# Optimization experiments

Hardware: AMD Instinct MI355X
Metric: run time of the kernel (lower is better)

The kernel has to match this reference:

```python
import jax, jax.numpy as jnp
import numpy as np

N = 100000          # nodes
E = 800000          # edges
H = 32              # hidden_features
L = 4               # num_layers
HS = 32             # hidden_edge_scores
EPS_BN = 1e-5
EPS_AGG = 1e-6


def _bn(x, g, b):
    # training-mode batch norm over the node/edge (batch) axis
    mu = jnp.mean(x, axis=0)
    var = jnp.var(x, axis=0)
    return (x - mu) * jax.lax.rsqrt(var + EPS_BN) * g + b


def setup_inputs() -> dict:
    key = jax.random.key(0)
    ks = jax.random.split(key, 24)
    rn = lambda k, s, sc=0.1: jax.random.normal(k, s, dtype=jnp.float32) * sc
    return {
        "x": rn(ks[0], (N, 1), 1.0),
        "e": rn(ks[1], (E, 1), 1.0),
        "edge_index": jax.random.randint(ks[2], (2, E), 0, N),
        # input projections
        "pe_w": rn(ks[3], (1, H)), "pe_b": rn(ks[4], (H,)),
        "ed_w": rn(ks[5], (1, H)), "ed_b": rn(ks[6], (H,)),
        # per-layer GatedGCN weights, stacked over layers
        "A_w": rn(ks[7], (L, H, H)), "A_b": rn(ks[8], (L, H)),
        "B_w": rn(ks[9], (L, H, H)), "B_b": rn(ks[10], (L, H)),
        "C_w": rn(ks[11], (L, H, H)), "C_b": rn(ks[12], (L, H)),
        "U_w": rn(ks[13], (L, H, H)), "U_b": rn(ks[14], (L, H)),
        "V_w": rn(ks[15], (L, H, H)), "V_b": rn(ks[16], (L, H)),
        # batch-norm affine params
        "bn_h_g": jnp.ones((L, H), jnp.float32), "bn_h_b": jnp.zeros((L, H), jnp.float32),
        "bn_e_g": jnp.ones((L, H), jnp.float32), "bn_e_b": jnp.zeros((L, H), jnp.float32),
        # score predictor: concat(src_h, dst_h, e) -> HS -> 1
        "W1_w": rn(ks[17], (3 * H, HS)), "W1_b": rn(ks[18], (HS,)),
        "W2_w": rn(ks[19], (HS, 1)), "W2_b": rn(ks[20], (1,)),
    }


def reference(x, e, edge_index, pe_w, pe_b, ed_w, ed_b,
              A_w, A_b, B_w, B_b, C_w, C_b, U_w, U_b, V_w, V_b,
              bn_h_g, bn_h_b, bn_e_g, bn_e_b, W1_w, W1_b, W2_w, W2_b):
    src, dst = edge_index[0], edge_index[1]
    h = x @ pe_w + pe_b          # [N, H]
    e = e @ ed_w + ed_b          # [E, H]
    n = h.shape[0]
    for l in range(L):
        Ah = h @ A_w[l] + A_b[l]
        Bh = h @ B_w[l] + B_b[l]
        Ce = e @ C_w[l] + C_b[l]
        Uh = h @ U_w[l] + U_b[l]
        Vh = h @ V_w[l] + V_b[l]
        # edge update: gather node features to edges
        e_new = Ah[dst] + Bh[src] + Ce               # [E, H]
        sigma = jax.nn.sigmoid(e_new)                # edge gates
        # gated mean aggregation: scatter-add to dst nodes
        num = jax.ops.segment_sum(sigma * Vh[src], dst, num_segments=n)
        den = jax.ops.segment_sum(sigma, dst, num_segments=n)
        h_new = Uh + num / (den + EPS_AGG)           # [N, H]
        # BN -> ReLU -> residual
        h = h + jax.nn.relu(_bn(h_new, bn_h_g[l], bn_h_b[l]))
        e = e + jax.nn.relu(_bn(e_new, bn_e_g[l], bn_e_b[l]))
    # score predictor over edges
    z = jnp.concatenate([h[src], h[dst], e], axis=1)  # [E, 3H]
    scores = jax.nn.relu(z @ W1_w + W1_b) @ W2_w + W2_b  # [E, 1]
    return scores
```

## Files before the change

### kernel.cpp

```cpp
#include <hip/hip_runtime.h>
#include <hip/hip_bf16.h>
#include <hip/hip_fp16.h>

#define NLAYERS 4
#define GRID_STRIDE 2048

typedef _Float16 half8_t __attribute__((ext_vector_type(8)));
typedef float float4_t __attribute__((ext_vector_type(4)));
typedef float float8_t __attribute__((ext_vector_type(8)));
typedef unsigned uint2_t __attribute__((ext_vector_type(2)));

__device__ __forceinline__ int permcol(int pos) { return (pos >> 1) | ((pos & 1) << 4); }

__device__ __forceinline__ void unp4v(uint2_t r, float* f)
{
    unsigned lo = r.x, hi = r.y;
    float2 a = __half22float2(*(__half2*)&lo);
    float2 b = __half22float2(*(__half2*)&hi);
    f[0] = a.x; f[1] = a.y; f[2] = b.x; f[3] = b.y;
}

__device__ __forceinline__ float fast_sigmoid(float x)
{
    return __builtin_amdgcn_rcpf(1.f + __expf(-x));
}

__global__ void zero_ints(int* __restrict__ p, int n)
{
    int i = blockIdx.x * 256 + threadIdx.x;
    if (i < n) p[i] = 0;
}

__global__ void hist_kernel(const int* __restrict__ dsts, int* __restrict__ counts, int E)
{
    int i = blockIdx.x * 256 + threadIdx.x;
    if (i < E) atomicAdd(&counts[dsts[i]], 1);
}

__global__ __launch_bounds__(256) void scan1(const int* __restrict__ counts,
                                             int* __restrict__ offsets,
                                             int* __restrict__ blocksums, int N)
{
    __shared__ int sdata[256];
    int t = threadIdx.x;
    int bbase = blockIdx.x * 1024;
    int v[4]; int s = 0;
#pragma unroll
    for (int q = 0; q < 4; q++) {
        int idx = bbase + t * 4 + q;
        v[q] = (idx < N) ? counts[idx] : 0;
        s += v[q];
    }
    sdata[t] = s;
    __syncthreads();
    for (int off = 1; off < 256; off <<= 1) {
        int x = (t >= off) ? sdata[t - off] : 0;
        __syncthreads();
        sdata[t] += x;
        __syncthreads();
    }
    int excl = sdata[t] - s;
    int run = excl;
#pragma unroll
    for (int q = 0; q < 4; q++) {
        int idx = bbase + t * 4 + q;
        if (idx < N) offsets[idx] = run;
        run += v[q];
    }
    if (t == 255) blocksums[blockIdx.x] = sdata[255];
}

__global__ void scan2(int* __restrict__ blocksums, int nb)
{
    if (threadIdx.x == 0 && blockIdx.x == 0) {
        int run = 0;
        for (int b = 0; b < nb; b++) { int t = blocksums[b]; blocksums[b] = run; run += t; }
    }
}

__global__ void scan3(int* __restrict__ offsets, const int* __restrict__ blocksums,
                      int* __restrict__ cursor, int N)
{
    int i = blockIdx.x * 256 + threadIdx.x;
    if (i < N) {
        int v = offsets[i] + blocksums[i >> 10];
        offsets[i] = v;
        cursor[i] = v;
    }
}

__global__ void scatter_perm(const int* __restrict__ dsts, int* __restrict__ cursor,
                             int* __restrict__ perm, int E, int N)
{
    int g = blockIdx.x & 7;
    int lo = (int)((long long)N * g >> 3);
    int hi = (int)((long long)N * (g + 1) >> 3);
    int nbg = gridDim.x >> 3;
    int bg = blockIdx.x >> 3;
    for (int i = bg * 256 + threadIdx.x; i < E; i += nbg * 256) {
        int d = dsts[i];
        if (d >= lo && d < hi) {
            int slot = atomicAdd(&cursor[d], 1);
            perm[slot] = i;
        }
    }
}

__global__ void gather_sd(const int* __restrict__ perm, const int* __restrict__ srcs,
                          const int* __restrict__ dsts, int* __restrict__ srcp,
                          int* __restrict__ dstp, int E)
{
    int i = blockIdx.x * 256 + threadIdx.x;
    if (i < E) {
        int e = perm[i];
        srcp[i] = srcs[e];
        dstp[i] = dsts[e];
    }
}

__global__ void init_proj4(const float* __restrict__ in, const float* __restrict__ w,
                           const float* __restrict__ b, float4* __restrict__ out, size_t n4)
{
    size_t i = (size_t)blockIdx.x * 256 + threadIdx.x;
    if (i < n4) {
        int j4 = (int)(i & 7) * 4;
        float xv = in[i >> 3];
        int c0 = permcol(j4), c1 = permcol(j4 + 1), c2 = permcol(j4 + 2), c3 = permcol(j4 + 3);
        out[i] = make_float4(fmaf(xv, w[c0], b[c0]), fmaf(xv, w[c1], b[c1]),
                             fmaf(xv, w[c2], b[c2]), fmaf(xv, w[c3], b[c3]));
    }
}

__global__ void init_ep16(const float* __restrict__ e_in, const int* __restrict__ perm,
                          const float* __restrict__ w, const float* __restrict__ b,
                          __half2* __restrict__ out, size_t n4)
{
    size_t i = (size_t)blockIdx.x * 256 + threadIdx.x;
    if (i < n4) {
        int row = (int)(i >> 3);
        float xv = e_in[perm[row]];
        int j4 = (int)(i & 7) * 4;
        int c0 = permcol(j4), c1 = permcol(j4 + 1), c2 = permcol(j4 + 2), c3 = permcol(j4 + 3);
        out[i * 2]     = __floats2half2_rn(fmaf(xv, w[c0], b[c0]), fmaf(xv, w[c1], b[c1]));
        out[i * 2 + 1] = __floats2half2_rn(fmaf(xv, w[c2], b[c2]), fmaf(xv, w[c3], b[c3]));
    }
}

template <int FUSE>
__global__ __launch_bounds__(256) void node_gemm(
    float* __restrict__ h, const float* __restrict__ hnew_in,
    const float* __restrict__ sc_h, const float* __restrict__ sh_h,
    const float* __restrict__ Aw, const float* __restrict__ Ab,
    const float* __restrict__ Bw, const float* __restrict__ Bb,
    const float* __restrict__ Uw, const float* __restrict__ Ub,
    const float* __restrict__ Vw, const float* __restrict__ Vb,
    __half* __restrict__ Ahh, __half* __restrict__ Bhh,
    float* __restrict__ Uhh, __half* __restrict__ Vhh, int N)
{
    int tid = threadIdx.x;
    int lane = tid & 63;
    int m = lane & 15, q = lane >> 4;
    half8_t bA0, bA1, bB0, bB1, bU0, bU1, bV0, bV1;
    float scq[8], shq[8];
#pragma unroll
    for (int i = 0; i < 8; i++) {
        int k = q * 8 + i;
        int kr = permcol(k);
        bA0[i] = (_Float16)Aw[kr * 32 + m];  bA1[i] = (_Float16)Aw[kr * 32 + m + 16];
        bB0[i] = (_Float16)Bw[kr * 32 + m];  bB1[i] = (_Float16)Bw[kr * 32 + m + 16];
        bU0[i] = (_Float16)Uw[kr * 32 + m];  bU1[i] = (_Float16)Uw[kr * 32 + m + 16];
        bV0[i] = (_Float16)Vw[kr * 32 + m];  bV1[i] = (_Float16)Vw[kr * 32 + m + 16];
        if (FUSE) { scq[i] = sc_h[k]; shq[i] = sh_h[k]; }
    }
    float ab0 = Ab[m], ab1 = Ab[m + 16];
    float bb0 = Bb[m], bb1 = Bb[m + 16];
    float ub0 = Ub[m], ub1 = Ub[m + 16];
    float vb0 = Vb[m], vb1 = Vb[m + 16];

    int ntile = (N + 15) >> 4;
    int wid = blockIdx.x * 4 + (tid >> 6);
    int nwave = gridDim.x * 4;
    for (int t = wid; t < ntile; t += nwave) {
        int base = t << 4;
        int arow = base + m;
        bool valid = arow < N;
        if (!valid) arow = N - 1;
        float8_t hv = *(const float8_t*)(h + (size_t)arow * 32 + q * 8);
        if (FUSE) {
            float8_t pv = *(const float8_t*)(hnew_in + (size_t)arow * 32 + q * 8);
#pragma unroll
            for (int i = 0; i < 8; i++)
                hv[i] += fmaxf(fmaf(pv[i], scq[i], shq[i]), 0.f);
            if (valid) *(float8_t*)(h + (size_t)arow * 32 + q * 8) = hv;
        }
        half8_t a;
#pragma unroll
        for (int i = 0; i < 8; i++) a[i] = (_Float16)hv[i];
        float4_t aA0 = __builtin_amdgcn_mfma_f32_16x16x32_f16(a, bA0, (float4_t){0,0,0,0}, 0, 0, 0);
        float4_t aA1 = __builtin_amdgcn_mfma_f32_16x16x32_f16(a, bA1, (float4_t){0,0,0,0}, 0, 0, 0);
        float4_t aB0 = __builtin_amdgcn_mfma_f32_16x16x32_f16(a, bB0, (float4_t){0,0,0,0}, 0, 0, 0);
        float4_t aB1 = __builtin_amdgcn_mfma_f32_16x16x32_f16(a, bB1, (float4_t){0,0,0,0}, 0, 0, 0);
        float4_t aU0 = __builtin_amdgcn_mfma_f32_16x16x32_f16(a, bU0, (float4_t){0,0,0,0}, 0, 0, 0);
        float4_t aU1 = __builtin_amdgcn_mfma_f32_16x16x32_f16(a, bU1, (float4_t){0,0,0,0}, 0, 0, 0);
        float4_t aV0 = __builtin_amdgcn_mfma_f32_16x16x32_f16(a, bV0, (float4_t){0,0,0,0}, 0, 0, 0);
        float4_t aV1 = __builtin_amdgcn_mfma_f32_16x16x32_f16(a, bV1, (float4_t){0,0,0,0}, 0, 0, 0);
#pragma unroll
        for (int reg = 0; reg < 4; reg++) {
            int node = base + q * 4 + reg;
            if (node < N) {
                size_t o = (size_t)node * 32;
                *(__half2*)(Ahh + o + 2 * m) = __floats2half2_rn(aA0[reg] + ab0, aA1[reg] + ab1);
                *(__half2*)(Bhh + o + 2 * m) = __floats2half2_rn(aB0[reg] + bb0, aB1[reg] + bb1);
                *(__half2*)(Vhh + o + 2 * m) = __floats2half2_rn(aV0[reg] + vb0, aV1[reg] + vb1);
                *(float2*)(Uhh + o + 2 * m)  = make_float2(aU0[reg] + ub0, aU1[reg] + ub1);
            }
        }
    }
}

template <int FIRST>
__global__ __launch_bounds__(256) void edge_en(
    __half* __restrict__ ep, __half* __restrict__ enh,
    const int* __restrict__ srcp, const int* __restrict__ dstp,
    const __half* __restrict__ Ah, const __half* __restrict__ Bh,
    const float* __restrict__ Cw, const float* __restrict__ Cb,
    const float* __restrict__ sc_e, const float* __restrict__ sh_e,
    float* __restrict__ partial, int E)
{
    __shared__ float red[256];
    int tid = threadIdx.x;
    int lane = tid & 63;
    int m = lane & 15, q = lane >> 4;
    half8_t b0, b1;
    float sca[8], sha[8];
#pragma unroll
    for (int i = 0; i < 8; i++) {
        int k = q * 8 + i;
        int kr = permcol(k);
        b0[i] = (_Float16)Cw[kr * 32 + m];
        b1[i] = (_Float16)Cw[kr * 32 + m + 16];
        if (!FIRST) { sca[i] = sc_e[k]; sha[i] = sh_e[k]; }
    }
    float cb0 = Cb[m], cb1 = Cb[m + 16];
    float es0 = 0.f, eq0 = 0.f, es1 = 0.f, eq1 = 0.f;

    int ntile = (E + 15) >> 4;
    int wid = blockIdx.x * 4 + (tid >> 6);
    int nwave = gridDim.x * 4;
    for (int t = wid; t < ntile; t += nwave) {
        int base = t << 4;
        int arow = base + m;
        bool avalid = arow < E;
        int ar = avalid ? arow : E - 1;
        half8_t a = __builtin_nontemporal_load(
            reinterpret_cast<const half8_t*>(ep + (size_t)ar * 32 + q * 8));
        if (!FIRST) {
            half8_t enp = __builtin_nontemporal_load(
                reinterpret_cast<const half8_t*>(enh + (size_t)ar * 32 + q * 8));
#pragma unroll
            for (int i = 0; i < 8; i++) {
                float ev = (float)a[i] + fmaxf(fmaf((float)enp[i], sca[i], sha[i]), 0.f);
                a[i] = (_Float16)ev;
            }
            if (avalid)
                __builtin_nontemporal_store(a,
                    reinterpret_cast<half8_t*>(ep + (size_t)ar * 32 + q * 8));
        }
        float4_t acc0 = __builtin_amdgcn_mfma_f32_16x16x32_f16(a, b0, (float4_t){0.f,0.f,0.f,0.f}, 0, 0, 0);
        float4_t acc1 = __builtin_amdgcn_mfma_f32_16x16x32_f16(a, b1, (float4_t){0.f,0.f,0.f,0.f}, 0, 0, 0);
#pragma unroll
        for (int reg = 0; reg < 4; reg++) {
            int row = q * 4 + reg;
            int edge = base + row;
            if (edge < E) {
                int s = srcp[edge], d = dstp[edge];
                float2 ah = __half22float2(*(const __half2*)(Ah + (size_t)d * 32 + 2 * m));
                float2 bh = __half22float2(*(const __half2*)(Bh + (size_t)s * 32 + 2 * m));
                float en0 = acc0[reg] + cb0 + ah.x + bh.x;
                float en1 = acc1[reg] + cb1 + ah.y + bh.y;
                __half2 env = __floats2half2_rn(en0, en1);
                unsigned enu = *(unsigned*)&env;
                __builtin_nontemporal_store(enu,
                    reinterpret_cast<unsigned*>(enh + (size_t)edge * 32 + 2 * m));
                es0 += en0; eq0 += en0 * en0;
                es1 += en1; eq1 += en1 * en1;
            }
        }
    }
    float* p = partial + (size_t)blockIdx.x * 64;
    __syncthreads();
    red[tid] = es0;
    __syncthreads();
    if (tid < 16) {
        float s = 0.f;
#pragma unroll
        for (int w = 0; w < 4; w++)
#pragma unroll
            for (int k = 0; k < 4; k++) s += red[w * 64 + k * 16 + tid];
        p[2 * tid] = s;
    }
    __syncthreads();
    red[tid] = es1;
    __syncthreads();
    if (tid < 16) {
        float s = 0.f;
#pragma unroll
        for (int w = 0; w < 4; w++)
#pragma unroll
            for (int k = 0; k < 4; k++) s += red[w * 64 + k * 16 + tid];
        p[2 * tid + 1] = s;
    }
    __syncthreads();
    red[tid] = eq0;
    __syncthreads();
    if (tid < 16) {
        float s = 0.f;
#pragma unroll
        for (int w = 0; w < 4; w++)
#pragma unroll
            for (int k = 0; k < 4; k++) s += red[w * 64 + k * 16 + tid];
        p[32 + 2 * tid] = s;
    }
    __syncthreads();
    red[tid] = eq1;
    __syncthreads();
    if (tid < 16) {
        float s = 0.f;
#pragma unroll
        for (int w = 0; w < 4; w++)
#pragma unroll
            for (int k = 0; k < 4; k++) s += red[w * 64 + k * 16 + tid];
        p[32 + 2 * tid + 1] = s;
    }
}

__global__ __launch_bounds__(256) void node_agg(
    const __half* __restrict__ enh, const int* __restrict__ srcp,
    const int* __restrict__ offsets, const int* __restrict__ counts,
    const __half* __restrict__ Vh, float* __restrict__ hnew,
    float* __restrict__ partial, int N)
{
    __shared__ float red[512];
    int tid = threadIdx.x, u = tid & 7, grp = tid >> 3;
    int c0 = 4 * u;
    float hs[4] = {0.f, 0.f, 0.f, 0.f}, hq[4] = {0.f, 0.f, 0.f, 0.f};

    for (int nb0 = blockIdx.x * 32; nb0 < N; nb0 += gridDim.x * 32) {
        int node = nb0 + grp;
        if (node >= N) break;
        int start = offsets[node], len = counts[node];
        float num[4] = {0.f, 0.f, 0.f, 0.f}, den[4] = {0.f, 0.f, 0.f, 0.f};
        int qq = 0;
        for (; qq + 2 <= len; qq += 2) {
            int p0 = start + qq, p1 = p0 + 1;
            int s0 = srcp[p0], s1 = srcp[p1];
            uint2_t enr0 = __builtin_nontemporal_load(
                reinterpret_cast<const uint2_t*>(enh + (size_t)p0 * 32 + c0));
            uint2_t enr1 = __builtin_nontemporal_load(
                reinterpret_cast<const uint2_t*>(enh + (size_t)p1 * 32 + c0));
            uint2_t vhr0 = *(const uint2_t*)(Vh + (size_t)s0 * 32 + c0);
            uint2_t vhr1 = *(const uint2_t*)(Vh + (size_t)s1 * 32 + c0);
            float en0[4], en1[4], vh0[4], vh1[4];
            unp4v(enr0, en0); unp4v(enr1, en1);
            unp4v(vhr0, vh0); unp4v(vhr1, vh1);
#pragma unroll
            for (int k = 0; k < 4; k++) {
                float sg0 = fast_sigmoid(en0[k]);
                float sg1 = fast_sigmoid(en1[k]);
                num[k] = fmaf(sg0, vh0[k], num[k]);
                num[k] = fmaf(sg1, vh1[k], num[k]);
                den[k] += sg0 + sg1;
            }
        }
        if (qq < len) {
            int p0 = start + qq;
            int s0 = srcp[p0];
            uint2_t enr0 = __builtin_nontemporal_load(
                reinterpret_cast<const uint2_t*>(enh + (size_t)p0 * 32 + c0));
            uint2_t vhr0 = *(const uint2_t*)(Vh + (size_t)s0 * 32 + c0);
            float en0[4], vh0[4];
            unp4v(enr0, en0); unp4v(vhr0, vh0);
#pragma unroll
            for (int k = 0; k < 4; k++) {
                float sg0 = fast_sigmoid(en0[k]);
                num[k] = fmaf(sg0, vh0[k], num[k]);
                den[k] += sg0;
            }
        }
        size_t ho = (size_t)node * 32 + c0;
        float4 uh = *(const float4*)(hnew + ho);
        float hv[4];
#pragma unroll
        for (int k = 0; k < 4; k++) {
            float* up = (float*)&uh;
            hv[k] = up[k] + num[k] * __builtin_amdgcn_rcpf(den[k] + 1e-6f);
        }
        *(float4*)(hnew + ho) = make_float4(hv[0], hv[1], hv[2], hv[3]);
#pragma unroll
        for (int k = 0; k < 4; k++) { hs[k] += hv[k]; hq[k] += hv[k] * hv[k]; }
    }

    float* p = partial + (size_t)blockIdx.x * 64;
#pragma unroll
    for (int k = 0; k < 4; k++) {
        __syncthreads();
        red[tid] = hs[k]; red[256 + tid] = hq[k];
        __syncthreads();
        if (tid < 8) {
            float s = 0.f;
#pragma unroll
            for (int g = 0; g < 32; g++) s += red[g * 8 + tid];
            p[4 * tid + k] = s;
        } else if (tid < 16) {
            int uu = tid - 8;
            float s = 0.f;
#pragma unroll
            for (int g = 0; g < 32; g++) s += red[256 + g * 8 + uu];
            p[32 + 4 * uu + k] = s;
        }
    }
}

__global__ __launch_bounds__(256) void stats_both(
    const float* __restrict__ pe, const float* __restrict__ ph, int nrows,
    double cntE, double cntN,
    const float* __restrict__ eg, const float* __restrict__ eb,
    const float* __restrict__ hg, const float* __restrict__ hb,
    float* __restrict__ stats)
{
    int j = blockIdx.x;
    int side = j >> 5, jj = j & 31;
    int col = (jj >> 1) | ((jj & 1) << 4);
    const float* partial = side ? ph : pe;
    __shared__ double rs[256], rq[256];
    double s = 0.0, q = 0.0;
    for (int r = threadIdx.x; r < nrows; r += 256) {
        s += (double)partial[(size_t)r * 64 + jj];
        q += (double)partial[(size_t)r * 64 + 32 + jj];
    }
    rs[threadIdx.x] = s; rq[threadIdx.x] = q;
    __syncthreads();
    for (int off = 128; off; off >>= 1) {
        if (threadIdx.x < off) { rs[threadIdx.x] += rs[threadIdx.x + off]; rq[threadIdx.x] += rq[threadIdx.x + off]; }
        __syncthreads();
    }
    if (threadIdx.x == 0) {
        double cnt = side ? cntN : cntE;
        double mean = rs[0] / cnt;
        double var = rq[0] / cnt - mean * mean;
        const float* g = side ? hg : eg;
        const float* b = side ? hb : eb;
        float scale = g[col] * (float)(1.0 / sqrt(var + 1e-5));
        int off2 = side ? 0 : 64;
        stats[off2 + jj] = scale;
        stats[off2 + 32 + jj] = b[col] - (float)mean * scale;
    }
}

__global__ void apply4_h16(const float4* __restrict__ pre, const float* __restrict__ scale,
                           const float* __restrict__ shift, const float4* __restrict__ hold,
                           __half2* __restrict__ h16, size_t n4)
{
    size_t i = (size_t)blockIdx.x * 256 + threadIdx.x;
    if (i < n4) {
        int j4 = (int)(i & 7) * 4;
        float4 sc = *(const float4*)(scale + j4);
        float4 sh = *(const float4*)(shift + j4);
        float4 p = pre[i], a = hold[i];
        a.x += fmaxf(fmaf(p.x, sc.x, sh.x), 0.f);
        a.y += fmaxf(fmaf(p.y, sc.y, sh.y), 0.f);
        a.z += fmaxf(fmaf(p.z, sc.z, sh.z), 0.f);
        a.w += fmaxf(fmaf(p.w, sc.w, sh.w), 0.f);
        h16[i * 2]     = __floats2half2_rn(a.x, a.y);
        h16[i * 2 + 1] = __floats2half2_rn(a.z, a.w);
    }
}

__global__ __launch_bounds__(256) void predictor(
    const __half* __restrict__ h16, const __half* __restrict__ ep,
    const __half* __restrict__ enh,
    const int* __restrict__ srcp, const int* __restrict__ dstp, const int* __restrict__ perm,
    const float* __restrict__ sc_e, const float* __restrict__ sh_e,
    const float* __restrict__ W1, const float* __restrict__ b1,
    const float* __restrict__ W2, const float* __restrict__ b2v,
    float* __restrict__ out, int E)
{
    int tid = threadIdx.x;
    int lane = tid & 63;
    int m = lane & 15, q = lane >> 4;
    half8_t bf00, bf01, bf10, bf11, bf20, bf21;
    float scq[8], shq[8];
#pragma unroll
    for (int i = 0; i < 8; i++) {
        int k = q * 8 + i;
        int kr = permcol(k);
        bf00[i] = (_Float16)W1[kr * 32 + m];
        bf01[i] = (_Float16)W1[kr * 32 + m + 16];
        bf10[i] = (_Float16)W1[(32 + kr) * 32 + m];
        bf11[i] = (_Float16)W1[(32 + kr) * 32 + m + 16];
        bf20[i] = (_Float16)W1[(64 + kr) * 32 + m];
        bf21[i] = (_Float16)W1[(64 + kr) * 32 + m + 16];
        scq[i] = sc_e[k]; shq[i] = sh_e[k];
    }
    float b10 = b1[m], b11 = b1[m + 16];
    float w20 = W2[m], w21 = W2[m + 16];
    float b2 = b2v[0];

    int ntile = (E + 15) >> 4;
    int wid = blockIdx.x * 4 + (tid >> 6);
    int nwave = gridDim.x * 4;
    for (int t = wid; t < ntile; t += nwave) {
        int base = t << 4;
        int arow = base + m;
        if (arow >= E) arow = E - 1;
        int s = srcp[arow], d = dstp[arow];
        half8_t a0 = *(const half8_t*)(h16 + (size_t)s * 32 + q * 8);
        half8_t a1 = *(const half8_t*)(h16 + (size_t)d * 32 + q * 8);
        half8_t ee = __builtin_nontemporal_load(
            reinterpret_cast<const half8_t*>(ep + (size_t)arow * 32 + q * 8));
        half8_t enr = __builtin_nontemporal_load(
            reinterpret_cast<const half8_t*>(enh + (size_t)arow * 32 + q * 8));
        half8_t a2;
#pragma unroll
        for (int i = 0; i < 8; i++) {
            float evv = (float)ee[i] + fmaxf(fmaf((float)enr[i], scq[i], shq[i]), 0.f);
            a2[i] = (_Float16)evv;
        }
        float4_t acc0 = {0.f, 0.f, 0.f, 0.f}, acc1 = {0.f, 0.f, 0.f, 0.f};
        acc0 = __builtin_amdgcn_mfma_f32_16x16x32_f16(a0, bf00, acc0, 0, 0, 0);
        acc1 = __builtin_amdgcn_mfma_f32_16x16x32_f16(a0, bf01, acc1, 0, 0, 0);
        acc0 = __builtin_amdgcn_mfma_f32_16x16x32_f16(a1, bf10, acc0, 0, 0, 0);
        acc1 = __builtin_amdgcn_mfma_f32_16x16x32_f16(a1, bf11, acc1, 0, 0, 0);
        acc0 = __builtin_amdgcn_mfma_f32_16x16x32_f16(a2, bf20, acc0, 0, 0, 0);
        acc1 = __builtin_amdgcn_mfma_f32_16x16x32_f16(a2, bf21, acc1, 0, 0, 0);
#pragma unroll
        for (int reg = 0; reg < 4; reg++) {
            float tp = fmaxf(acc0[reg] + b10, 0.f) * w20
                     + fmaxf(acc1[reg] + b11, 0.f) * w21;
            tp += __shfl_xor(tp, 1);
            tp += __shfl_xor(tp, 2);
            tp += __shfl_xor(tp, 4);
            tp += __shfl_xor(tp, 8);
            int idx = base + q * 4 + reg;
            if (m == 0 && idx < E) {
                int oe = perm[idx];
                out[oe] = tp + b2;
            }
        }
    }
}

extern "C" void kernel_launch(void* const* d_in, const int* in_sizes, int n_in,
                              void* d_out, int out_size, void* d_ws, size_t ws_size,
                              hipStream_t stream)
{
    const int N = in_sizes[0];
    const int E = in_sizes[1];

    const float* x    = (const float*)d_in[0];
    const float* e_in = (const float*)d_in[1];
    const int*   eidx = (const int*)d_in[2];
    const float* pe_w = (const float*)d_in[3];
    const float* pe_b = (const float*)d_in[4];
    const float* ed_w = (const float*)d_in[5];
    const float* ed_b = (const float*)d_in[6];
    const float* Aw = (const float*)d_in[7];
    const float* Ab = (const float*)d_in[8];
    const float* Bw = (const float*)d_in[9];
    const float* Bb = (const float*)d_in[10];
    const float* Cw = (const float*)d_in[11];
    const float* Cb = (const float*)d_in[12];
    const float* Uw = (const float*)d_in[13];
    const float* Ub = (const float*)d_in[14];
    const float* Vw = (const float*)d_in[15];
    const float* Vb = (const float*)d_in[16];
    const float* bn_h_g = (const float*)d_in[17];
    const float* bn_h_b = (const float*)d_in[18];
    const float* bn_e_g = (const float*)d_in[19];
    const float* bn_e_b = (const float*)d_in[20];
    const float* W1w = (const float*)d_in[21];
    const float* W1b = (const float*)d_in[22];
    const float* W2w = (const float*)d_in[23];
    const float* W2b = (const float*)d_in[24];

    const int* srcs = eidx;
    const int* dsts = eidx + E;

    size_t nh = (size_t)N * 32;
    size_t eh = (size_t)E * 32;

    float* ws = (float*)d_ws;
    float* stats     = ws;
    float* partial_h = stats + 128;
    float* partial_e = partial_h + GRID_STRIDE * 64;
    float* h    = partial_e + GRID_STRIDE * 64;
    float* hnew = h + nh;
    __half* Ah  = (__half*)(hnew + nh);
    __half* Bh  = Ah + nh;
    __half* Vh  = Bh + nh;
    __half* ep  = Vh + nh;
    __half* enh = ep + eh;
    int* counts    = (int*)(enh + eh);
    int* offsets   = counts + N;
    int* cursor    = offsets + N;
    int* blocksums = cursor + N;
    int* perm      = blocksums + 128;
    int* srcp      = perm + E;
    int* dstp      = srcp + E;

    size_t nh4 = nh / 4, eh4 = eh / 4;
    int gh4 = (int)((nh4 + 255) / 256);
    int ge4 = (int)((eh4 + 255) / 256);
    int gN = (N + 255) / 256;
    int gE = (E + 255) / 256;
    int nb = (N + 1023) / 1024;
    int ntileN = (N + 15) / 16;
    int gGemm = (ntileN + 3) / 4;
    if (gGemm > GRID_STRIDE) gGemm = GRID_STRIDE;

    zero_ints<<<gN, 256, 0, stream>>>(counts, N);
    hist_kernel<<<gE, 256, 0, stream>>>(dsts, counts, E);
    scan1<<<nb, 256, 0, stream>>>(counts, offsets, blocksums, N);
    scan2<<<1, 64, 0, stream>>>(blocksums, nb);
    scan3<<<gN, 256, 0, stream>>>(offsets, blocksums, cursor, N);
    scatter_perm<<<GRID_STRIDE, 256, 0, stream>>>(dsts, cursor, perm, E, N);
    gather_sd<<<gE, 256, 0, stream>>>(perm, srcs, dsts, srcp, dstp, E);

    init_proj4<<<gh4, 256, 0, stream>>>(x, pe_w, pe_b, (float4*)h, nh4);
    init_ep16<<<ge4, 256, 0, stream>>>(e_in, perm, ed_w, ed_b, (__half2*)ep, eh4);

    for (int l = 0; l < NLAYERS; l++) {
        if (l == 0)
            node_gemm<0><<<gGemm, 256, 0, stream>>>(h, hnew, stats + 0, stats + 32,
                Aw + l * 1024, Ab + l * 32, Bw + l * 1024, Bb + l * 32,
                Uw + l * 1024, Ub + l * 32, Vw + l * 1024, Vb + l * 32,
                Ah, Bh, hnew, Vh, N);
        else
            node_gemm<1><<<gGemm, 256, 0, stream>>>(h, hnew, stats + 0, stats + 32,
                Aw + l * 1024, Ab + l * 32, Bw + l * 1024, Bb + l * 32,
                Uw + l * 1024, Ub + l * 32, Vw + l * 1024, Vb + l * 32,
                Ah, Bh, hnew, Vh, N);
        if (l == 0)
            edge_en<1><<<GRID_STRIDE, 256, 0, stream>>>(ep, enh, srcp, dstp, Ah, Bh,
                Cw + l * 1024, Cb + l * 32, stats + 64, stats + 96, partial_e, E);
        else
            edge_en<0><<<GRID_STRIDE, 256, 0, stream>>>(ep, enh, srcp, dstp, Ah, Bh,
                Cw + l * 1024, Cb + l * 32, stats + 64, stats + 96, partial_e, E);
        node_agg<<<GRID_STRIDE, 256, 0, stream>>>(enh, srcp, offsets, counts,
            Vh, hnew, partial_h, N);
        stats_both<<<64, 256, 0, stream>>>(partial_e, partial_h, GRID_STRIDE,
            (double)E, (double)N,
            bn_e_g + l * 32, bn_e_b + l * 32, bn_h_g + l * 32, bn_h_b + l * 32, stats);
    }

    apply4_h16<<<gh4, 256, 0, stream>>>((const float4*)hnew, stats + 0, stats + 32,
                                        (const float4*)h, (__half2*)Ah, nh4);

    predictor<<<GRID_STRIDE, 256, 0, stream>>>((const __half*)Ah, ep, enh,
                                               srcp, dstp, perm, stats + 64, stats + 96,
                                               W1w, W1b, W2w, W2b,
                                               (float*)d_out, E);
}
```

Before: 759.0 us.

## Fuse edge update and node aggregation into one dst-partitioned kernel using LDS

Merges the edge_en and node_agg kernels into a single edge_layer kernel. Each block owns 32 destination nodes and their contiguous dst-sorted edge range, computes the new edge features, and stages up to CAP edges plus their source indices in LDS. The aggregation then reads from LDS, falling back to global memory for edges beyond CAP. This removes one launch and most of the global re-read of enh, at the cost of about 23KB of LDS per block (lower occupancy) and load imbalance from varying node degrees. Nontemporal loads and stores are also replaced with plain accesses.

After: 689.5 us. 9.2% less time.

```diff
diff --git a/kernel.cpp b/kernel.cpp
--- a/kernel.cpp
+++ b/kernel.cpp
@@ -4,6 +4,8 @@
 
 #define NLAYERS 4
 #define GRID_STRIDE 2048
+#define NB 32
+#define CAP 352
 
 typedef _Float16 half8_t __attribute__((ext_vector_type(8)));
 typedef float float4_t __attribute__((ext_vector_type(4)));
@@ -219,18 +221,30 @@
 }
 
 template <int FIRST>
-__global__ __launch_bounds__(256) void edge_en(
+__global__ __launch_bounds__(256) void edge_layer(
     __half* __restrict__ ep, __half* __restrict__ enh,
     const int* __restrict__ srcp, const int* __restrict__ dstp,
+    const int* __restrict__ offsets, const int* __restrict__ counts,
     const __half* __restrict__ Ah, const __half* __restrict__ Bh,
+    const __half* __restrict__ Vh, float* __restrict__ hnew,
     const float* __restrict__ Cw, const float* __restrict__ Cb,
     const float* __restrict__ sc_e, const float* __restrict__ sh_e,
-    float* __restrict__ partial, int E)
-{
-    __shared__ float red[256];
+    float* __restrict__ partial_e, float* __restrict__ partial_h,
+    int N, int E)
+{
+    __shared__ __half en_lds[CAP * 32];
+    __shared__ int src_lds[CAP];
+    __shared__ float red[512];
+
     int tid = threadIdx.x;
     int lane = tid & 63;
     int m = lane & 15, q = lane >> 4;
+
+    int n0 = blockIdx.x * NB;
+    int n1 = n0 + NB; if (n1 > N) n1 = N;
+    int e0 = offsets[n0];
+    int e1 = (n1 < N) ? offsets[n1] : E;
+
     half8_t b0, b1;
     float sca[8], sha[8];
 #pragma unroll
@@ -244,60 +258,59 @@
     float cb0 = Cb[m], cb1 = Cb[m + 16];
     float es0 = 0.f, eq0 = 0.f, es1 = 0.f, eq1 = 0.f;
 
-    int ntile = (E + 15) >> 4;
-    int wid = blockIdx.x * 4 + (tid >> 6);
-    int nwave = gridDim.x * 4;
-    for (int t = wid; t < ntile; t += nwave) {
-        int base = t << 4;
-        int arow = base + m;
-        bool avalid = arow < E;
-        int ar = avalid ? arow : E - 1;
-        half8_t a = __builtin_nontemporal_load(
-            reinterpret_cast<const half8_t*>(ep + (size_t)ar * 32 + q * 8));
+    int len = e1 - e0;
+    int T = (len + 15) >> 4;
+    int w = tid >> 6;
+    for (int t = w; t < T; t += 4) {
+        int eb = e0 + (t << 4);
+        int arow = eb + m;
+        bool avalid = arow < e1;
+        int ar = avalid ? arow : e1 - 1;
+        half8_t a = *(const half8_t*)(ep + (size_t)ar * 32 + q * 8);
         if (!FIRST) {
-            half8_t enp = __builtin_nontemporal_load(
-                reinterpret_cast<const half8_t*>(enh + (size_t)ar * 32 + q * 8));
+            half8_t enp = *(const half8_t*)(enh + (size_t)ar * 32 + q * 8);
 #pragma unroll
             for (int i = 0; i < 8; i++) {
                 float ev = (float)a[i] + fmaxf(fmaf((float)enp[i], sca[i], sha[i]), 0.f);
                 a[i] = (_Float16)ev;
             }
-            if (avalid)
-                __builtin_nontemporal_store(a,
-                    reinterpret_cast<half8_t*>(ep + (size_t)ar * 32 + q * 8));
+            if (avalid) *(half8_t*)(ep + (size_t)ar * 32 + q * 8) = a;
         }
         float4_t acc0 = __builtin_amdgcn_mfma_f32_16x16x32_f16(a, b0, (float4_t){0.f,0.f,0.f,0.f}, 0, 0, 0);
         float4_t acc1 = __builtin_amdgcn_mfma_f32_16x16x32_f16(a, b1, (float4_t){0.f,0.f,0.f,0.f}, 0, 0, 0);
 #pragma unroll
         for (int reg = 0; reg < 4; reg++) {
-            int row = q * 4 + reg;
-            int edge = base + row;
-            if (edge < E) {
+            int edge = eb + q * 4 + reg;
+            if (edge < e1) {
                 int s = srcp[edge], d = dstp[edge];
                 float2 ah = __half22float2(*(const __half2*)(Ah + (size_t)d * 32 + 2 * m));
                 float2 bh = __half22float2(*(const __half2*)(Bh + (size_t)s * 32 + 2 * m));
                 float en0 = acc0[reg] + cb0 + ah.x + bh.x;
                 float en1 = acc1[reg] + cb1 + ah.y + bh.y;
                 __half2 env = __floats2half2_rn(en0, en1);
-                unsigned enu = *(unsigned*)&env;
-                __builtin_nontemporal_store(enu,
-                    reinterpret_cast<unsigned*>(enh + (size_t)edge * 32 + 2 * m));
+                *(__half2*)(enh + (size_t)edge * 32 + 2 * m) = env;
+                int le = edge - e0;
+                if (le < CAP) {
+                    *(__half2*)(en_lds + le * 32 + 2 * m) = env;
+                    if (m == 0) src_lds[le] = s;
+                }
                 es0 += en0; eq0 += en0 * en0;
                 es1 += en1; eq1 += en1 * en1;
             }
         }
     }
-    float* p = partial + (size_t)blockIdx.x * 64;
+
+    float* pe = partial_e + (size_t)blockIdx.x * 64;
     __syncthreads();
     red[tid] = es0;
     __syncthreads();
     if (tid < 16) {
         float s = 0.f;
 #pragma unroll
-        for (int w = 0; w < 4; w++)
-#pragma unroll
-            for (int k = 0; k < 4; k++) s += red[w * 64 + k * 16 + tid];
-        p[2 * tid] = s;
+        for (int ww = 0; ww < 4; ww++)
+#pragma unroll
+            for (int k = 0; k < 4; k++) s += red[ww * 64 + k * 16 + tid];
+        pe[2 * tid] = s;
     }
     __syncthreads();
     red[tid] = es1;
@@ -305,10 +318,10 @@
     if (tid < 16) {
         float s = 0.f;
 #pragma unroll
-        for (int w = 0; w < 4; w++)
-#pragma unroll
-            for (int k = 0; k < 4; k++) s += red[w * 64 + k * 16 + tid];
-        p[2 * tid + 1] = s;
+        for (int ww = 0; ww < 4; ww++)
+#pragma unroll
+            for (int k = 0; k < 4; k++) s += red[ww * 64 + k * 16 + tid];
+        pe[2 * tid + 1] = s;
     }
     __syncthreads();
     red[tid] = eq0;
@@ -316,10 +329,10 @@
     if (tid < 16) {
         float s = 0.f;
 #pragma unroll
-        for (int w = 0; w < 4; w++)
-#pragma unroll
-            for (int k = 0; k < 4; k++) s += red[w * 64 + k * 16 + tid];
-        p[32 + 2 * tid] = s;
+        for (int ww = 0; ww < 4; ww++)
+#pragma unroll
+            for (int k = 0; k < 4; k++) s += red[ww * 64 + k * 16 + tid];
+        pe[32 + 2 * tid] = s;
     }
     __syncthreads();
     red[tid] = eq1;
@@ -327,37 +340,28 @@
     if (tid < 16) {
         float s = 0.f;
 #pragma unroll
-        for (int w = 0; w < 4; w++)
-#pragma unroll
-            for (int k = 0; k < 4; k++) s += red[w * 64 + k * 16 + tid];
-        p[32 + 2 * tid + 1] = s;
-    }
-}
-
-__global__ __launch_bounds__(256) void node_agg(
-    const __half* __restrict__ enh, const int* __restrict__ srcp,
-    const int* __restrict__ offsets, const int* __restrict__ counts,
-    const __half* __restrict__ Vh, float* __restrict__ hnew,
-    float* __restrict__ partial, int N)
-{
-    __shared__ float red[512];
-    int tid = threadIdx.x, u = tid & 7, grp = tid >> 3;
+        for (int ww = 0; ww < 4; ww++)
+#pragma unroll
+            for (int k = 0; k < 4; k++) s += red[ww * 64 + k * 16 + tid];
+        pe[32 + 2 * tid + 1] = s;
+    }
+
+    int u = tid & 7, grp = tid >> 3;
     int c0 = 4 * u;
     float hs[4] = {0.f, 0.f, 0.f, 0.f}, hq[4] = {0.f, 0.f, 0.f, 0.f};
 
-    for (int nb0 = blockIdx.x * 32; nb0 < N; nb0 += gridDim.x * 32) {
-        int node = nb0 + grp;
-        if (node >= N) break;
-        int start = offsets[node], len = counts[node];
+    int n = n0 + grp;
+    if (n < N) {
+        int start = offsets[n], lenn = counts[n];
+        int lb = start - e0;
+        int inl = CAP - lb; if (inl < 0) inl = 0; if (inl > lenn) inl = lenn;
         float num[4] = {0.f, 0.f, 0.f, 0.f}, den[4] = {0.f, 0.f, 0.f, 0.f};
         int qq = 0;
-        for (; qq + 2 <= len; qq += 2) {
-            int p0 = start + qq, p1 = p0 + 1;
-            int s0 = srcp[p0], s1 = srcp[p1];
-            uint2_t enr0 = __builtin_nontemporal_load(
-                reinterpret_cast<const uint2_t*>(enh + (size_t)p0 * 32 + c0));
-            uint2_t enr1 = __builtin_nontemporal_load(
-                reinterpret_cast<const uint2_t*>(enh + (size_t)p1 * 32 + c0));
+        for (; qq + 2 <= inl; qq += 2) {
+            int le0 = lb + qq, le1 = le0 + 1;
+            int s0 = src_lds[le0], s1 = src_lds[le1];
+            uint2_t enr0 = *(const uint2_t*)(en_lds + le0 * 32 + c0);
+            uint2_t enr1 = *(const uint2_t*)(en_lds + le1 * 32 + c0);
             uint2_t vhr0 = *(const uint2_t*)(Vh + (size_t)s0 * 32 + c0);
             uint2_t vhr1 = *(const uint2_t*)(Vh + (size_t)s1 * 32 + c0);
             float en0[4], en1[4], vh0[4], vh1[4];
@@ -372,11 +376,10 @@
                 den[k] += sg0 + sg1;
             }
         }
-        if (qq < len) {
-            int p0 = start + qq;
-            int s0 = srcp[p0];
-            uint2_t enr0 = __builtin_nontemporal_load(
-                reinterpret_cast<const uint2_t*>(enh + (size_t)p0 * 32 + c0));
+        if (qq < inl) {
+            int le0 = lb + qq;
+            int s0 = src_lds[le0];
+            uint2_t enr0 = *(const uint2_t*)(en_lds + le0 * 32 + c0);
             uint2_t vhr0 = *(const uint2_t*)(Vh + (size_t)s0 * 32 + c0);
             float en0[4], vh0[4];
             unp4v(enr0, en0); unp4v(vhr0, vh0);
@@ -386,8 +389,23 @@
                 num[k] = fmaf(sg0, vh0[k], num[k]);
                 den[k] += sg0;
             }
-        }
-        size_t ho = (size_t)node * 32 + c0;
+            qq++;
+        }
+        for (; qq < lenn; qq++) {
+            int ge = start + qq;
+            int s0 = srcp[ge];
+            uint2_t enr0 = *(const uint2_t*)(enh + (size_t)ge * 32 + c0);
+            uint2_t vhr0 = *(const uint2_t*)(Vh + (size_t)s0 * 32 + c0);
+            float en0[4], vh0[4];
+            unp4v(enr0, en0); unp4v(vhr0, vh0);
+#pragma unroll
+            for (int k = 0; k < 4; k++) {
+                float sg0 = fast_sigmoid(en0[k]);
+                num[k] = fmaf(sg0, vh0[k], num[k]);
+                den[k] += sg0;
+            }
+        }
+        size_t ho = (size_t)n * 32 + c0;
         float4 uh = *(const float4*)(hnew + ho);
         float hv[4];
 #pragma unroll
@@ -400,7 +418,7 @@
         for (int k = 0; k < 4; k++) { hs[k] += hv[k]; hq[k] += hv[k] * hv[k]; }
     }
 
-    float* p = partial + (size_t)blockIdx.x * 64;
+    float* ph = partial_h + (size_t)blockIdx.x * 64;
 #pragma unroll
     for (int k = 0; k < 4; k++) {
         __syncthreads();
@@ -410,13 +428,13 @@
             float s = 0.f;
 #pragma unroll
             for (int g = 0; g < 32; g++) s += red[g * 8 + tid];
-            p[4 * tid + k] = s;
+            ph[4 * tid + k] = s;
         } else if (tid < 16) {
             int uu = tid - 8;
             float s = 0.f;
 #pragma unroll
             for (int g = 0; g < 32; g++) s += red[256 + g * 8 + uu];
-            p[32 + 4 * uu + k] = s;
+            ph[32 + 4 * uu + k] = s;
         }
     }
 }
@@ -516,10 +534,8 @@
         int s = srcp[arow], d = dstp[arow];
         half8_t a0 = *(const half8_t*)(h16 + (size_t)s * 32 + q * 8);
         half8_t a1 = *(const half8_t*)(h16 + (size_t)d * 32 + q * 8);
-        half8_t ee = __builtin_nontemporal_load(
-            reinterpret_cast<const half8_t*>(ep + (size_t)arow * 32 + q * 8));
-        half8_t enr = __builtin_nontemporal_load(
-            reinterpret_cast<const half8_t*>(enh + (size_t)arow * 32 + q * 8));
+        half8_t ee = *(const half8_t*)(ep + (size_t)arow * 32 + q * 8);
+        half8_t enr = *(const half8_t*)(enh + (size_t)arow * 32 + q * 8);
         half8_t a2;
 #pragma unroll
         for (int i = 0; i < 8; i++) {
@@ -588,12 +604,13 @@
 
     size_t nh = (size_t)N * 32;
     size_t eh = (size_t)E * 32;
+    int nbE = (N + NB - 1) / NB;
 
     float* ws = (float*)d_ws;
     float* stats     = ws;
-    float* partial_h = stats + 128;
-    float* partial_e = partial_h + GRID_STRIDE * 64;
-    float* h    = partial_e + GRID_STRIDE * 64;
+    float* partial_e = stats + 128;
+    float* partial_h = partial_e + (size_t)nbE * 64;
+    float* h    = partial_h + (size_t)nbE * 64;
     float* hnew = h + nh;
     __half* Ah  = (__half*)(hnew + nh);
     __half* Bh  = Ah + nh;
@@ -641,14 +658,14 @@
                 Uw + l * 1024, Ub + l * 32, Vw + l * 1024, Vb + l * 32,
                 Ah, Bh, hnew, Vh, N);
         if (l == 0)
-            edge_en<1><<<GRID_STRIDE, 256, 0, stream>>>(ep, enh, srcp, dstp, Ah, Bh,
-                Cw + l * 1024, Cb + l * 32, stats + 64, stats + 96, partial_e, E);
+            edge_layer<1><<<nbE, 256, 0, stream>>>(ep, enh, srcp, dstp, offsets, counts,
+                Ah, Bh, Vh, hnew, Cw + l * 1024, Cb + l * 32,
+                stats + 64, stats + 96, partial_e, partial_h, N, E);
         else
-            edge_en<0><<<GRID_STRIDE, 256, 0, stream>>>(ep, enh, srcp, dstp, Ah, Bh,
-                Cw + l * 1024, Cb + l * 32, stats + 64, stats + 96, partial_e, E);
-        node_agg<<<GRID_STRIDE, 256, 0, stream>>>(enh, srcp, offsets, counts,
-            Vh, hnew, partial_h, N);
-        stats_both<<<64, 256, 0, stream>>>(partial_e, partial_h, GRID_STRIDE,
+            edge_layer<0><<<nbE, 256, 0, stream>>>(ep, enh, srcp, dstp, offsets, counts,
+                Ah, Bh, Vh, hnew, Cw + l * 1024, Cb + l * 32,
+                stats + 64, stats + 96, partial_e, partial_h, N, E);
+        stats_both<<<64, 256, 0, stream>>>(partial_e, partial_h, nbE,
             (double)E, (double)N,
             bn_e_g + l * 32, bn_e_b + l * 32, bn_h_g + l * 32, bn_h_b + l * 32, stats);
     }
```
